# Kernel tuning notes

Measured on AMD Instinct MI355X. Metric: run time of the kernel, lower is better.

Reference implementation:

```python
import jax, jax.numpy as jnp
import numpy as np

N_NODES = 100000
N_EDGES = 1600000
N_GRAPHS = 512


def gcn_conv(x, src, dst, W, b, n_nodes):
    """PyG GCNConv: add self-loops, symmetric norm, linear, scatter-add, bias."""
    h = x @ W.T                                   # [N, out]
    ones = jnp.ones(src.shape[0], dtype=x.dtype)
    deg = jax.ops.segment_sum(ones, dst, num_segments=n_nodes)   # in-degree incl. self-loops
    dinv = jnp.where(deg > 0, jax.lax.rsqrt(deg), 0.0)
    norm = dinv[src] * dinv[dst]                  # [E+N]
    msg = h[src] * norm[:, None]                  # gather + scale
    out = jax.ops.segment_sum(msg, dst, num_segments=n_nodes)
    return out + b


def setup_inputs() -> dict:
    key = jax.random.key(0)
    ks = jax.random.split(key, 8)
    x = jax.random.normal(ks[0], (N_NODES, 2), dtype=jnp.float32)
    edge_index = jax.random.randint(ks[1], (2, N_EDGES), 0, N_NODES, dtype=jnp.int64)
    batch = jnp.sort(jax.random.randint(ks[2], (N_NODES,), 0, N_GRAPHS, dtype=jnp.int64))
    def glorot(k, shape):
        lim = jnp.sqrt(6.0 / (shape[0] + shape[1])).astype(jnp.float32)
        return jax.random.uniform(k, shape, jnp.float32, -lim, lim)
    return {
        "x": x, "edge_index": edge_index, "batch": batch,
        "W1": glorot(ks[3], (32, 2)),  "b1": jnp.zeros(32, jnp.float32),
        "W2": glorot(ks[4], (64, 32)), "b2": jnp.zeros(64, jnp.float32),
        "W3": glorot(ks[5], (32, 64)), "b3": jnp.zeros(32, jnp.float32),
        "Wfc": glorot(ks[6], (1, 32)), "bfc": jnp.zeros(1, jnp.float32),
    }


def reference(x, edge_index, batch, W1, b1, W2, b2, W3, b3, Wfc, bfc):
    n = x.shape[0]
    loop = jnp.arange(n, dtype=edge_index.dtype)
    src = jnp.concatenate([edge_index[0], loop])  # self-loops appended once
    dst = jnp.concatenate([edge_index[1], loop])

    h = jax.nn.relu(gcn_conv(x, src, dst, W1, b1, n))   # dropout = identity (eval)
    h = jax.nn.relu(gcn_conv(h, src, dst, W2, b2, n))
    h = jax.nn.relu(gcn_conv(h, src, dst, W3, b3, n))

    # global_mean_pool over graph ids
    sums = jax.ops.segment_sum(h, batch, num_segments=N_GRAPHS)
    cnts = jax.ops.segment_sum(jnp.ones((n,), h.dtype), batch, num_segments=N_GRAPHS)
    pooled = sums / jnp.maximum(cnts, 1.0)[:, None]     # [G, 32]
    return pooled @ Wfc.T + bfc                         # [G, 1]
```

## Files before the change

### kernel.cpp

```cpp
#include <hip/hip_runtime.h>
#include <hip/hip_fp16.h>


static constexpr int TPB = 256;
static constexpr int NB1 = 256;
static constexpr int NB_SCAN = 256;
static constexpr int P2CAP = 6144;

__global__ void p1_hist_gptr_kernel(const int* __restrict__ dst, int* __restrict__ hist,
                                    int E, int chunk, int shift, int B,
                                    const int* __restrict__ batch, int* __restrict__ gstart,
                                    int n, int G) {
  int b = blockIdx.x, t = threadIdx.x;
  if (b >= NB1) {
    int i = (b - NB1) * TPB + t;
    if (i >= n) return;
    int bb = batch[i];
    int bp = (i == 0) ? -1 : batch[i - 1];
    for (int g = bp + 1; g <= bb; ++g) gstart[g] = i;
    if (i == n - 1)
      for (int g = bb + 1; g <= G; ++g) gstart[g] = n;
    return;
  }
  __shared__ int h[1024];
  for (int i = t; i < B; i += TPB) h[i] = 0;
  __syncthreads();
  int lo = b * chunk, hi = min(lo + chunk, E);
  for (int e = lo + t; e < hi; e += TPB) atomicAdd(&h[dst[e] >> shift], 1);
  __syncthreads();
  for (int i = t; i < B; i += TPB) hist[i * NB1 + b] = h[i];
}

__global__ void scan_partial_kernel(const int* __restrict__ a, int* __restrict__ bsum,
                                    int n, int seg) {
  int b = blockIdx.x, t = threadIdx.x;
  int lo = b * seg, hi = min(lo + seg, n);
  int acc = 0;
  for (int i = lo + t; i < hi; i += TPB) acc += a[i];
  __shared__ int red[TPB];
  red[t] = acc;
  __syncthreads();
  for (int st = TPB / 2; st > 0; st >>= 1) {
    if (t < st) red[t] += red[t + st];
    __syncthreads();
  }
  if (t == 0) bsum[b] = red[0];
}

__global__ void scan_emit_kernel(int* __restrict__ a, const int* __restrict__ bsum,
                                 int n, int seg) {
  int b = blockIdx.x, t = threadIdx.x;
  int lo = b * seg, hi = min(lo + seg, n);
  __shared__ int cs[TPB];
  __shared__ int s_run;
  cs[t] = (t < b) ? bsum[t] : 0;
  __syncthreads();
  for (int st = TPB / 2; st > 0; st >>= 1) {
    if (t < st) cs[t] += cs[t + st];
    __syncthreads();
  }
  if (t == 0) s_run = cs[0];
  __syncthreads();
  for (int base = lo; base < hi; base += TPB) {
    int i = base + t;
    int v = (i < hi) ? a[i] : 0;
    cs[t] = v;
    __syncthreads();
    for (int off = 1; off < TPB; off <<= 1) {
      int u = (t >= off) ? cs[t - off] : 0;
      __syncthreads();
      cs[t] += u;
      __syncthreads();
    }
    if (i < hi) a[i] = s_run + cs[t] - v;
    __syncthreads();
    if (t == 0) s_run += cs[TPB - 1];
    __syncthreads();
  }
}

__global__ void p1_scatter_kernel(const int* __restrict__ src, const int* __restrict__ dst,
                                  const int* __restrict__ hist, unsigned int* __restrict__ epk,
                                  int E, int chunk, int shift, int srcbits, int B) {
  __shared__ int cur[1024];
  int b = blockIdx.x, t = threadIdx.x;
  for (int i = t; i < B; i += TPB) cur[i] = hist[i * NB1 + b];
  __syncthreads();
  int lo = b * chunk, hi = min(lo + chunk, E);
  int span1 = (1 << shift) - 1;
  for (int e = lo + t; e < hi; e += TPB) {
    int d = dst[e];
    int pos = atomicAdd(&cur[d >> shift], 1);
    epk[pos] = ((unsigned int)(d & span1) << srcbits) | (unsigned int)src[e];
  }
}

__global__ __launch_bounds__(TPB) void p2_sort_kernel(
    const unsigned int* __restrict__ epk, const int* __restrict__ hist,
    const float2* __restrict__ x2,
    int* __restrict__ rowptr, float* __restrict__ dinv, float2* __restrict__ u0,
    int* __restrict__ esrc, int N, int E, int shift, int srcbits, int B) {
  int bkt = blockIdx.x, t = threadIdx.x;
  int span = 1 << shift;
  unsigned int smask = (1u << srcbits) - 1u;
  int nb = bkt << shift;
  int bstart = hist[bkt * NB1];
  int bend = (bkt + 1 < B) ? hist[(bkt + 1) * NB1] : E;
  int bsize = bend - bstart;
  __shared__ int cnt[256];
  __shared__ int ex[256];
  __shared__ int ldata[P2CAP];
  __shared__ int lsrc[P2CAP];
  bool stage = (bsize <= P2CAP);
  if (t < span) cnt[t] = 0;
  __syncthreads();
  if (stage) {
    for (int i = t; i < bsize; i += TPB) ldata[i] = (int)epk[bstart + i];
    __syncthreads();
    for (int i = t; i < bsize; i += TPB)
      atomicAdd(&cnt[((unsigned int)ldata[i]) >> srcbits], 1);
  } else {
    for (int e = bstart + t; e < bend; e += TPB) atomicAdd(&cnt[epk[e] >> srcbits], 1);
  }
  __syncthreads();
  int v = (t < span) ? cnt[t] : 0;
  ex[t] = v;
  __syncthreads();
  for (int off = 1; off < 256; off <<= 1) {
    int u = (t >= off) ? ex[t - off] : 0;
    __syncthreads();
    ex[t] += u;
    __syncthreads();
  }
  int excl = ex[t] - v;
  int node = nb + t;
  if (t < span && node < N) {
    rowptr[node] = bstart + excl;
    float dv = rsqrtf((float)v + 1.0f);
    dinv[node] = dv;
    float2 xv = x2[node];
    u0[node] = make_float2(xv.x * dv, xv.y * dv);
  }
  if (bkt == 0 && t == 0) rowptr[N] = E;
  __syncthreads();
  if (t < span) cnt[t] = stage ? excl : bstart + excl;
  __syncthreads();
  if (stage) {
    for (int i = t; i < bsize; i += TPB) {
      unsigned int p = (unsigned int)ldata[i];
      int pos = atomicAdd(&cnt[p >> srcbits], 1);
      lsrc[pos] = (int)(p & smask);
    }
    __syncthreads();
    for (int i = t; i < bsize; i += TPB) esrc[bstart + i] = lsrc[i];
  } else {
    for (int e = bstart + t; e < bend; e += TPB) {
      unsigned int p = epk[e];
      int pos = atomicAdd(&cnt[p >> srcbits], 1);
      esrc[pos] = (int)(p & smask);
    }
  }
}

__global__ void layer1_kernel(const float2* __restrict__ u0, const int* __restrict__ rowptr,
                              const int* __restrict__ esrc, const float* __restrict__ W1,
                              const float* __restrict__ b1, const float* __restrict__ dinv,
                              __half* __restrict__ u1_16, int n) {
  int tid = blockIdx.x * blockDim.x + threadIdx.x;
  int i = tid >> 2, split = tid & 3;
  if (i >= n) return;
  float ax = 0.f, ay = 0.f;
  if (split == 0) {
    float2 s = u0[i];
    ax = s.x; ay = s.y;
  }
  int r0 = rowptr[i], r1 = rowptr[i + 1];
  int e = r0 + split;
  while (e + 4 < r1) {
    int s0 = esrc[e], s1 = esrc[e + 4];
    float2 v0 = u0[s0];
    float2 v1 = u0[s1];
    ax += v0.x + v1.x;
    ay += v0.y + v1.y;
    e += 8;
  }
  if (e < r1) {
    float2 v = u0[esrc[e]];
    ax += v.x; ay += v.y;
  }
  ax += __shfl_xor(ax, 1, 64); ay += __shfl_xor(ay, 1, 64);
  ax += __shfl_xor(ax, 2, 64); ay += __shfl_xor(ay, 2, 64);
  float di = dinv[i];
  int f0 = split * 8;
  union { float4 f4[1]; __half h[8]; } oh;
#pragma unroll
  for (int k = 0; k < 8; ++k) {
    int f = f0 + k;
    float hv = fmaxf(di * (W1[f * 2 + 0] * ax + W1[f * 2 + 1] * ay) + b1[f], 0.f);
    oh.h[k] = __float2half(di * hv);
  }
  *(float4*)&u1_16[(size_t)i * 32 + f0] = oh.f4[0];
}

template <bool EPI>
__global__ void gather32_kernel(const float4* __restrict__ a16,
                                const int* __restrict__ rowptr, const int* __restrict__ esrc,
                                const float* __restrict__ dinv, const float* __restrict__ b,
                                float4* __restrict__ out16, int n) {
  int tid = blockIdx.x * blockDim.x + threadIdx.x;
  int i = tid >> 4;
  int sub = tid & 15;
  int split = sub >> 2, q = sub & 3;
  if (i >= n) return;
  float acc[8] = {0.f, 0.f, 0.f, 0.f, 0.f, 0.f, 0.f, 0.f};
  auto addrow = [&](int s) {
    union { float4 f4; __half2 h2[4]; } u;
    u.f4 = a16[(size_t)s * 4 + q];
    float2 a0 = __half22float2(u.h2[0]);
    float2 a1 = __half22float2(u.h2[1]);
    float2 a2 = __half22float2(u.h2[2]);
    float2 a3 = __half22float2(u.h2[3]);
    acc[0] += a0.x; acc[1] += a0.y; acc[2] += a1.x; acc[3] += a1.y;
    acc[4] += a2.x; acc[5] += a2.y; acc[6] += a3.x; acc[7] += a3.y;
  };
  if (split == 0) addrow(i);
  int r0 = rowptr[i], r1 = rowptr[i + 1];
  int e = r0 + split;
  while (e + 4 < r1) {
    int s0 = esrc[e], s1 = esrc[e + 4];
    addrow(s0);
    addrow(s1);
    e += 8;
  }
  if (e < r1) addrow(esrc[e]);
#pragma unroll
  for (int k = 0; k < 8; ++k) acc[k] += __shfl_xor(acc[k], 4, 64);
#pragma unroll
  for (int k = 0; k < 8; ++k) acc[k] += __shfl_xor(acc[k], 8, 64);
  if (split != 0) return;
  if (EPI) {
    float di = dinv[i];
    const float4 bv0 = ((const float4*)b)[2 * q];
    const float4 bv1 = ((const float4*)b)[2 * q + 1];
    acc[0] = fmaxf(di * acc[0] + bv0.x, 0.f);
    acc[1] = fmaxf(di * acc[1] + bv0.y, 0.f);
    acc[2] = fmaxf(di * acc[2] + bv0.z, 0.f);
    acc[3] = fmaxf(di * acc[3] + bv0.w, 0.f);
    acc[4] = fmaxf(di * acc[4] + bv1.x, 0.f);
    acc[5] = fmaxf(di * acc[5] + bv1.y, 0.f);
    acc[6] = fmaxf(di * acc[6] + bv1.z, 0.f);
    acc[7] = fmaxf(di * acc[7] + bv1.w, 0.f);
  }
  union { float4 f4; __half2 h2[4]; } o;
  o.h2[0] = __floats2half2_rn(acc[0], acc[1]);
  o.h2[1] = __floats2half2_rn(acc[2], acc[3]);
  o.h2[2] = __floats2half2_rn(acc[4], acc[5]);
  o.h2[3] = __floats2half2_rn(acc[6], acc[7]);
  out16[(size_t)i * 4 + q] = o.f4;
}

__global__ __launch_bounds__(TPB) void t2t3_kernel(
    const float4* __restrict__ U1h, const float* __restrict__ W2, const float* __restrict__ b2,
    const float* __restrict__ W3, const float* __restrict__ dinv,
    __half* __restrict__ g3_16, int n) {
  constexpr int SN = 136;
  __shared__ float U1l[32 * SN];
  __shared__ float h2l[64 * SN];
  __shared__ float W2l[32 * 68];
  __shared__ float W3l[64 * 36];
  __shared__ float dil[128];
  int t = threadIdx.x;
  int base = blockIdx.x * 128;
  for (int idx = t; idx < 2048; idx += TPB) {
    int k = idx >> 5, j = idx & 31;
    W2l[j * 68 + k] = W2[idx];
  }
  for (int idx = t; idx < 2048; idx += TPB) {
    int k = idx >> 6, j = idx & 63;
    W3l[j * 36 + k] = W3[idx];
  }
  if (t < 128) dil[t] = (base + t < n) ? dinv[base + t] : 0.f;
  for (int it = 0; it < 2; ++it) {
    int idx = it * 256 + t;
    int nl = idx >> 2, j0 = (idx & 3) * 8;
    int node = base + nl;
    union { float4 f4; __half2 h2[4]; } u;
    u.f4 = (node < n) ? U1h[(size_t)node * 4 + (idx & 3)]
                      : make_float4(0.f, 0.f, 0.f, 0.f);
#pragma unroll
    for (int k = 0; k < 4; ++k) {
      float2 p = __half22float2(u.h2[k]);
      U1l[(j0 + 2 * k + 0) * SN + nl] = p.x;
      U1l[(j0 + 2 * k + 1) * SN + nl] = p.y;
    }
  }
  __syncthreads();
  {
    int a = t & 15, bb = t >> 4;
    int n0 = a * 8, k0 = bb * 4;
    float acc[4][8];
#pragma unroll
    for (int kk = 0; kk < 4; ++kk)
#pragma unroll
      for (int nn = 0; nn < 8; ++nn) acc[kk][nn] = 0.f;
#pragma unroll 8
    for (int j = 0; j < 32; ++j) {
      float4 ua = *(const float4*)&U1l[j * SN + n0];
      float4 ub = *(const float4*)&U1l[j * SN + n0 + 4];
      float4 w = *(const float4*)&W2l[j * 68 + k0];
      float un[8] = {ua.x, ua.y, ua.z, ua.w, ub.x, ub.y, ub.z, ub.w};
      float wk[4] = {w.x, w.y, w.z, w.w};
#pragma unroll
      for (int kk = 0; kk < 4; ++kk)
#pragma unroll
        for (int nn = 0; nn < 8; ++nn) acc[kk][nn] += un[nn] * wk[kk];
    }
    float4 bv = ((const float4*)b2)[bb];
    float bk[4] = {bv.x, bv.y, bv.z, bv.w};
#pragma unroll
    for (int kk = 0; kk < 4; ++kk) {
      float o[8];
#pragma unroll
      for (int nn = 0; nn < 8; ++nn)
        o[nn] = fmaxf(dil[n0 + nn] * acc[kk][nn] + bk[kk], 0.f);
      *(float4*)&h2l[(k0 + kk) * SN + n0] = make_float4(o[0], o[1], o[2], o[3]);
      *(float4*)&h2l[(k0 + kk) * SN + n0 + 4] = make_float4(o[4], o[5], o[6], o[7]);
    }
  }
  __syncthreads();
  {
    int a = t & 15, bb = t >> 4;
    int n0 = a * 8, k0 = bb * 2;
    float acc[2][8];
#pragma unroll
    for (int kk = 0; kk < 2; ++kk)
#pragma unroll
      for (int nn = 0; nn < 8; ++nn) acc[kk][nn] = 0.f;
#pragma unroll 8
    for (int j = 0; j < 64; ++j) {
      float4 ua = *(const float4*)&h2l[j * SN + n0];
      float4 ub = *(const float4*)&h2l[j * SN + n0 + 4];
      float w0 = W3l[j * 36 + k0];
      float w1 = W3l[j * 36 + k0 + 1];
      float un[8] = {ua.x, ua.y, ua.z, ua.w, ub.x, ub.y, ub.z, ub.w};
#pragma unroll
      for (int nn = 0; nn < 8; ++nn) {
        acc[0][nn] += un[nn] * w0;
        acc[1][nn] += un[nn] * w1;
      }
    }
#pragma unroll
    for (int nn = 0; nn < 8; ++nn) {
      int node = base + n0 + nn;
      if (node < n) {
        float di = dil[n0 + nn];
        __half2 hv = __floats2half2_rn(di * acc[0][nn], di * acc[1][nn]);
        *(__half2*)&g3_16[(size_t)node * 32 + k0] = hv;
      }
    }
  }
}

__global__ void poolfc_kernel(const __half2* __restrict__ h3, const int* __restrict__ gstart,
                              const float* __restrict__ Wfc, const float* __restrict__ bfc,
                              float* __restrict__ out) {
  int gi = blockIdx.x;
  int s = gstart[gi], e = gstart[gi + 1];
  int t = threadIdx.x;
  int nl = t >> 4, f2 = t & 15;
  float ax = 0.f, ay = 0.f;
  for (int i = s + nl; i < e; i += 16) {
    float2 v = __half22float2(h3[(size_t)i * 16 + f2]);
    ax += v.x; ay += v.y;
  }
  __shared__ float redx[256], redy[256];
  redx[t] = ax; redy[t] = ay;
  __syncthreads();
  for (int st = 128; st >= 16; st >>= 1) {
    if (t < st) { redx[t] += redx[t + st]; redy[t] += redy[t + st]; }
    __syncthreads();
  }
  if (t < 16) {
    float cnt = fmaxf((float)(e - s), 1.f);
    float v = (redx[t] / cnt) * Wfc[2 * t] + (redy[t] / cnt) * Wfc[2 * t + 1];
    for (int o = 8; o; o >>= 1) v += __shfl_down(v, o, 16);
    if (t == 0) out[gi] = v + bfc[0];
  }
}

extern "C" void kernel_launch(void* const* d_in, const int* in_sizes, int n_in,
                              void* d_out, int out_size, void* d_ws, size_t ws_size,
                              hipStream_t stream) {
  const float* x     = (const float*)d_in[0];
  const int*   ei    = (const int*)d_in[1];
  const int*   batch = (const int*)d_in[2];
  const float* W1    = (const float*)d_in[3];
  const float* b1    = (const float*)d_in[4];
  const float* W2    = (const float*)d_in[5];
  const float* b2    = (const float*)d_in[6];
  const float* W3    = (const float*)d_in[7];
  const float* b3    = (const float*)d_in[8];
  const float* Wfc   = (const float*)d_in[9];
  const float* bfc   = (const float*)d_in[10];
  float* out = (float*)d_out;

  const int N = in_sizes[0] / 2;
  const int E = in_sizes[1] / 2;
  const int G = out_size;
  const int* src = ei;
  const int* dst = ei + E;

  int shift = 8;
  while ((((N + (1 << shift) - 1) >> shift)) > 1024) ++shift;
  const int B = (N + (1 << shift) - 1) >> shift;
  const int srcbits = 32 - shift;
  const int chunkE = (E + NB1 - 1) / NB1;
  const int M = B * NB1;
  const int segM = (M + NB_SCAN - 1) / NB_SCAN;

  char* ws = (char*)d_ws;
  size_t off = 0;
  auto alloc = [&](size_t bytes) -> char* {
    char* p = ws + off;
    off += (bytes + 255) & ~(size_t)255;
    return p;
  };
  float*        dinv   = (float*)alloc((size_t)N * 4);
  int*          rowptr = (int*)alloc((size_t)(N + 1) * 4);
  int*          esrc   = (int*)alloc((size_t)E * 4);
  int*          gstart = (int*)alloc((size_t)(G + 1) * 4);
  int*          hist   = (int*)alloc((size_t)M * 4);
  int*          bsum   = (int*)alloc((size_t)NB_SCAN * 4);
  unsigned int* epk    = (unsigned int*)alloc((size_t)E * 4);
  float2*       u0     = (float2*)alloc((size_t)N * 8);
  __half*       u1_16  = (__half*)alloc((size_t)N * 32 * 2);
  __half*       U1h    = (__half*)alloc((size_t)N * 32 * 2);
  __half*       g3_16  = (__half*)alloc((size_t)N * 32 * 2);
  __half*       hA16   = (__half*)alloc((size_t)N * 32 * 2);

  const int gptrBlocks = (N + TPB - 1) / TPB;
  p1_hist_gptr_kernel<<<NB1 + gptrBlocks, TPB, 0, stream>>>(dst, hist, E, chunkE, shift, B,
                                                            batch, gstart, N, G);
  scan_partial_kernel<<<NB_SCAN, TPB, 0, stream>>>(hist, bsum, M, segM);
  scan_emit_kernel<<<NB_SCAN, TPB, 0, stream>>>(hist, bsum, M, segM);
  p1_scatter_kernel<<<NB1, TPB, 0, stream>>>(src, dst, hist, epk, E, chunkE, shift, srcbits, B);
  p2_sort_kernel<<<B, TPB, 0, stream>>>(epk, hist, (const float2*)x, rowptr, dinv, u0, esrc,
                                        N, E, shift, srcbits, B);

  layer1_kernel<<<((size_t)N * 4 + TPB - 1) / TPB, TPB, 0, stream>>>(
      u0, rowptr, esrc, W1, b1, dinv, u1_16, N);

  gather32_kernel<false><<<((size_t)N * 16 + TPB - 1) / TPB, TPB, 0, stream>>>(
      (const float4*)u1_16, rowptr, esrc, dinv, b2, (float4*)U1h, N);
  t2t3_kernel<<<(N + 127) / 128, TPB, 0, stream>>>(
      (const float4*)U1h, W2, b2, W3, dinv, g3_16, N);

  gather32_kernel<true><<<((size_t)N * 16 + TPB - 1) / TPB, TPB, 0, stream>>>(
      (const float4*)g3_16, rowptr, esrc, dinv, b3, (float4*)hA16, N);

  poolfc_kernel<<<G, 256, 0, stream>>>((const __half2*)hA16, gstart, Wfc, bfc, out);
}
```

Baseline: 214.3 us.

## Split 32-wide gather features into two 16-feature halves for cache locality

```diff
diff --git a/kernel.cpp b/kernel.cpp
--- a/kernel.cpp
+++ b/kernel.cpp
@@ -199,23 +199,24 @@
     float hv = fmaxf(di * (W1[f * 2 + 0] * ax + W1[f * 2 + 1] * ay) + b1[f], 0.f);
     oh.h[k] = __float2half(di * hv);
   }
-  *(float4*)&u1_16[(size_t)i * 32 + f0] = oh.f4[0];
+  float4* dst = (float4*)(u1_16 + (size_t)(split >> 1) * n * 16);
+  dst[(size_t)i * 2 + (split & 1)] = oh.f4[0];
 }
 
 template <bool EPI>
-__global__ void gather32_kernel(const float4* __restrict__ a16,
+__global__ void gather16_kernel(const float4* __restrict__ a16h,
                                 const int* __restrict__ rowptr, const int* __restrict__ esrc,
                                 const float* __restrict__ dinv, const float* __restrict__ b,
-                                float4* __restrict__ out16, int n) {
+                                float4* __restrict__ out16, int n, int h) {
   int tid = blockIdx.x * blockDim.x + threadIdx.x;
-  int i = tid >> 4;
-  int sub = tid & 15;
-  int split = sub >> 2, q = sub & 3;
+  int i = tid >> 3;
+  int sub = tid & 7;
+  int split = sub >> 1, q = sub & 1;
   if (i >= n) return;
   float acc[8] = {0.f, 0.f, 0.f, 0.f, 0.f, 0.f, 0.f, 0.f};
   auto addrow = [&](int s) {
     union { float4 f4; __half2 h2[4]; } u;
-    u.f4 = a16[(size_t)s * 4 + q];
+    u.f4 = a16h[(size_t)s * 2 + q];
     float2 a0 = __half22float2(u.h2[0]);
     float2 a1 = __half22float2(u.h2[1]);
     float2 a2 = __half22float2(u.h2[2]);
@@ -234,14 +235,14 @@
   }
   if (e < r1) addrow(esrc[e]);
 #pragma unroll
+  for (int k = 0; k < 8; ++k) acc[k] += __shfl_xor(acc[k], 2, 64);
+#pragma unroll
   for (int k = 0; k < 8; ++k) acc[k] += __shfl_xor(acc[k], 4, 64);
-#pragma unroll
-  for (int k = 0; k < 8; ++k) acc[k] += __shfl_xor(acc[k], 8, 64);
   if (split != 0) return;
   if (EPI) {
     float di = dinv[i];
-    const float4 bv0 = ((const float4*)b)[2 * q];
-    const float4 bv1 = ((const float4*)b)[2 * q + 1];
+    const float4 bv0 = ((const float4*)b)[h * 4 + 2 * q];
+    const float4 bv1 = ((const float4*)b)[h * 4 + 2 * q + 1];
     acc[0] = fmaxf(di * acc[0] + bv0.x, 0.f);
     acc[1] = fmaxf(di * acc[1] + bv0.y, 0.f);
     acc[2] = fmaxf(di * acc[2] + bv0.z, 0.f);
@@ -256,7 +257,7 @@
   o.h2[1] = __floats2half2_rn(acc[2], acc[3]);
   o.h2[2] = __floats2half2_rn(acc[4], acc[5]);
   o.h2[3] = __floats2half2_rn(acc[6], acc[7]);
-  out16[(size_t)i * 4 + q] = o.f4;
+  out16[(size_t)i * 4 + h * 2 + q] = o.f4;
 }
 
 __global__ __launch_bounds__(TPB) void t2t3_kernel(
@@ -349,13 +350,14 @@
         acc[1][nn] += un[nn] * w1;
       }
     }
+    __half* gh = g3_16 + (size_t)(k0 >> 4) * (size_t)n * 16;
 #pragma unroll
     for (int nn = 0; nn < 8; ++nn) {
       int node = base + n0 + nn;
       if (node < n) {
         float di = dil[n0 + nn];
         __half2 hv = __floats2half2_rn(di * acc[0][nn], di * acc[1][nn]);
-        *(__half2*)&g3_16[(size_t)node * 32 + k0] = hv;
+        *(__half2*)&gh[(size_t)node * 16 + (k0 & 15)] = hv;
       }
     }
   }
@@ -450,13 +452,18 @@
   layer1_kernel<<<((size_t)N * 4 + TPB - 1) / TPB, TPB, 0, stream>>>(
       u0, rowptr, esrc, W1, b1, dinv, u1_16, N);
 
-  gather32_kernel<false><<<((size_t)N * 16 + TPB - 1) / TPB, TPB, 0, stream>>>(
-      (const float4*)u1_16, rowptr, esrc, dinv, b2, (float4*)U1h, N);
+  const int g16Blocks = ((size_t)N * 8 + TPB - 1) / TPB;
+  gather16_kernel<false><<<g16Blocks, TPB, 0, stream>>>(
+      (const float4*)u1_16, rowptr, esrc, dinv, b2, (float4*)U1h, N, 0);
+  gather16_kernel<false><<<g16Blocks, TPB, 0, stream>>>(
+      (const float4*)(u1_16 + (size_t)N * 16), rowptr, esrc, dinv, b2, (float4*)U1h, N, 1);
   t2t3_kernel<<<(N + 127) / 128, TPB, 0, stream>>>(
       (const float4*)U1h, W2, b2, W3, dinv, g3_16, N);
 
-  gather32_kernel<true><<<((size_t)N * 16 + TPB - 1) / TPB, TPB, 0, stream>>>(
-      (const float4*)g3_16, rowptr, esrc, dinv, b3, (float4*)hA16, N);
+  gather16_kernel<true><<<g16Blocks, TPB, 0, stream>>>(
+      (const float4*)g3_16, rowptr, esrc, dinv, b3, (float4*)hA16, N, 0);
+  gather16_kernel<true><<<g16Blocks, TPB, 0, stream>>>(
+      (const float4*)(g3_16 + (size_t)N * 16), rowptr, esrc, dinv, b3, (float4*)hA16, N, 1);
 
   poolfc_kernel<<<G, 256, 0, stream>>>((const __half2*)hA16, gstart, Wfc, bfc, out);
 }
```

After: 229.0 us. 6.9% more time.
